# Kernel optimization log

Hardware: AMD Instinct MI355X
Metric: run time of the kernel (lower is better)

Reference implementation:

```python
import jax, jax.numpy as jnp
import numpy as np


def setup_inputs() -> dict:
    key = jax.random.key(0)
    heatmaps = jax.random.normal(key, (16, 24, 64, 64, 64), dtype=jnp.float32)
    return {"heatmaps": heatmaps}


def reference(heatmaps) -> jnp.ndarray:
    N, J, D, H, W = heatmaps.shape
    # softmax over the flattened D*H*W volume per (n, j)
    p = jax.nn.softmax(heatmaps.reshape(N, J, D * H * W), axis=2).reshape(N, J, D, H, W)
    x_maps = p.sum(axis=(2, 3))  # (N, J, W)
    y_maps = p.sum(axis=(2, 4))  # (N, J, H)
    z_maps = p.sum(axis=(3, 4))  # (N, J, D)
    w_idx = jnp.arange(W, dtype=p.dtype)
    h_idx = jnp.arange(H, dtype=p.dtype)
    d_idx = jnp.arange(D, dtype=p.dtype)
    x_preds = (x_maps * w_idx).sum(axis=2) / W - 0.5
    y_preds = (y_maps * h_idx).sum(axis=2) / H - 0.5
    z_preds = (z_maps * d_idx).sum(axis=2) / D - 0.5
    return jnp.stack((x_preds, y_preds, z_preds), axis=2)  # (N, J, 3)
```

## Files before the change

kernel.cpp:

```cpp
#include <hip/hip_runtime.h>

#define NJ   384
#define VOL  262144
#define CHUNKS 16
#define BLOCK 256
#define ELEMS_PER_BLOCK (VOL / CHUNKS)
#define VEC4_PER_BLOCK  (ELEMS_PER_BLOCK/4)
#define ITERS (VEC4_PER_BLOCK / BLOCK)


__global__ void jir_zero(float* __restrict__ acc) {
    int i = blockIdx.x * blockDim.x + threadIdx.x;
    if (i < NJ * 4) acc[i] = 0.0f;
}

__global__ __launch_bounds__(BLOCK) void jir_accum(const float* __restrict__ hm,
                                                   float* __restrict__ acc) {
    const int slice = blockIdx.x >> 4;
    const int chunk = blockIdx.x & 15;
    const int t = threadIdx.x;

    const float4* __restrict__ base =
        (const float4*)(hm + (size_t)slice * VOL + (size_t)chunk * ELEMS_PER_BLOCK);
    const int fbase = chunk * ELEMS_PER_BLOCK;

    float S = 0.f, Sx = 0.f, Sy = 0.f, Sz = 0.f;

#pragma unroll
    for (int i = 0; i < ITERS; ++i) {
        const int v = i * BLOCK + t;
        const float4 q = base[v];
        const int f = fbase + (v << 2);
        const float e0 = expf(q.x);
        const float e1 = expf(q.y);
        const float e2 = expf(q.z);
        const float e3 = expf(q.w);
        const float Se = (e0 + e1) + (e2 + e3);
        const float w0 = (float)(f & 63);
        const float hh = (float)((f >> 6) & 63);
        const float dd = (float)(f >> 12);
        S  += Se;
        Sx += w0 * Se + (e1 + 2.0f * e2 + 3.0f * e3);
        Sy += hh * Se;
        Sz += dd * Se;
    }

#pragma unroll
    for (int off = 32; off > 0; off >>= 1) {
        S  += __shfl_down(S,  off, 64);
        Sx += __shfl_down(Sx, off, 64);
        Sy += __shfl_down(Sy, off, 64);
        Sz += __shfl_down(Sz, off, 64);
    }

    __shared__ float red[BLOCK / 64][4];
    const int wid  = t >> 6;
    const int lane = t & 63;
    if (lane == 0) {
        red[wid][0] = S; red[wid][1] = Sx; red[wid][2] = Sy; red[wid][3] = Sz;
    }
    __syncthreads();
    if (t < 4) {
        const float v = red[0][t] + red[1][t] + red[2][t] + red[3][t];
        atomicAdd(&acc[slice * 4 + t], v);
    }
}

__global__ void jir_finalize(const float* __restrict__ acc, float* __restrict__ out) {
    int s = blockIdx.x * blockDim.x + threadIdx.x;
    if (s < NJ) {
        const float S  = acc[s * 4 + 0];
        const float Sx = acc[s * 4 + 1];
        const float Sy = acc[s * 4 + 2];
        const float Sz = acc[s * 4 + 3];
        const float inv = 1.0f / S;
        const float scale = inv * (1.0f / 64.0f);
        out[s * 3 + 0] = Sx * scale - 0.5f;
        out[s * 3 + 1] = Sy * scale - 0.5f;
        out[s * 3 + 2] = Sz * scale - 0.5f;
    }
}

extern "C" void kernel_launch(void* const* d_in, const int* in_sizes, int n_in,
                              void* d_out, int out_size, void* d_ws, size_t ws_size,
                              hipStream_t stream) {
    const float* hm = (const float*)d_in[0];
    float* out = (float*)d_out;
    float* acc = (float*)d_ws;

    jir_zero<<<(NJ * 4 + 255) / 256, 256, 0, stream>>>(acc);
    jir_accum<<<NJ * CHUNKS, BLOCK, 0, stream>>>(hm, acc);
    jir_finalize<<<(NJ + 191) / 192, 192, 0, stream>>>(acc, out);
}
```

Measured before the change: 519.4 us.

## Replace atomics with per-block partials, drop zero kernel, use fast exp

Each block now writes its four partial sums to a per-block workspace slot instead of atomically adding into a zeroed accumulator. The finalize kernel then sums the 16 chunk partials for each slice, so the separate zero-fill launch goes away. The accumulation loop switches to the hardware-approximate __expf, derives the w/h/d coordinates from the thread index and iteration number instead of recomputing them from the flat offset, and uses explicit FMAs. The kernel streams about 400MB and is expected to be bandwidth-bound, so the savings are mostly one fewer launch and less ALU work, at some cost in exp accuracy.

```diff
diff --git a/kernel.cpp b/kernel.cpp
--- a/kernel.cpp
+++ b/kernel.cpp
@@ -1,48 +1,43 @@
 #include <hip/hip_runtime.h>
 
-#define NJ   384
-#define VOL  262144
+
+#define NJ     384
+#define VOL    262144
 #define CHUNKS 16
-#define BLOCK 256
-#define ELEMS_PER_BLOCK (VOL / CHUNKS)
-#define VEC4_PER_BLOCK  (ELEMS_PER_BLOCK/4)
-#define ITERS (VEC4_PER_BLOCK / BLOCK)
-
-
-__global__ void jir_zero(float* __restrict__ acc) {
-    int i = blockIdx.x * blockDim.x + threadIdx.x;
-    if (i < NJ * 4) acc[i] = 0.0f;
-}
+#define BLOCK  256
+#define EPB    (VOL / CHUNKS)
+#define ITERS  (EPB / 4 / BLOCK)
 
 __global__ __launch_bounds__(BLOCK) void jir_accum(const float* __restrict__ hm,
-                                                   float* __restrict__ acc) {
+                                                   float4* __restrict__ partial) {
     const int slice = blockIdx.x >> 4;
     const int chunk = blockIdx.x & 15;
     const int t = threadIdx.x;
 
     const float4* __restrict__ base =
-        (const float4*)(hm + (size_t)slice * VOL + (size_t)chunk * ELEMS_PER_BLOCK);
-    const int fbase = chunk * ELEMS_PER_BLOCK;
+        (const float4*)(hm + (size_t)slice * VOL + (size_t)chunk * EPB) + t;
+
+    const float w0    = (float)((t & 15) << 2);
+    const float hbase = (float)(t >> 4);
+    const float dbase = (float)(chunk << 2);
 
     float S = 0.f, Sx = 0.f, Sy = 0.f, Sz = 0.f;
 
 #pragma unroll
     for (int i = 0; i < ITERS; ++i) {
-        const int v = i * BLOCK + t;
-        const float4 q = base[v];
-        const int f = fbase + (v << 2);
-        const float e0 = expf(q.x);
-        const float e1 = expf(q.y);
-        const float e2 = expf(q.z);
-        const float e3 = expf(q.w);
+        const float4 q = base[i * BLOCK];
+        const float e0 = __expf(q.x);
+        const float e1 = __expf(q.y);
+        const float e2 = __expf(q.z);
+        const float e3 = __expf(q.w);
         const float Se = (e0 + e1) + (e2 + e3);
-        const float w0 = (float)(f & 63);
-        const float hh = (float)((f >> 6) & 63);
-        const float dd = (float)(f >> 12);
+        const float hh = hbase + (float)((i & 3) << 4);
+        const float dd = dbase + (float)(i >> 2);
+        const float cx = fmaf(3.0f, e3, fmaf(2.0f, e2, e1));
         S  += Se;
-        Sx += w0 * Se + (e1 + 2.0f * e2 + 3.0f * e3);
-        Sy += hh * Se;
-        Sz += dd * Se;
+        Sx += fmaf(w0, Se, cx);
+        Sy  = fmaf(hh, Se, Sy);
+        Sz  = fmaf(dd, Se, Sz);
     }
 
 #pragma unroll
@@ -60,21 +55,27 @@
         red[wid][0] = S; red[wid][1] = Sx; red[wid][2] = Sy; red[wid][3] = Sz;
     }
     __syncthreads();
-    if (t < 4) {
-        const float v = red[0][t] + red[1][t] + red[2][t] + red[3][t];
-        atomicAdd(&acc[slice * 4 + t], v);
+    if (t == 0) {
+        float4 p;
+        p.x = (red[0][0] + red[1][0]) + (red[2][0] + red[3][0]);
+        p.y = (red[0][1] + red[1][1]) + (red[2][1] + red[3][1]);
+        p.z = (red[0][2] + red[1][2]) + (red[2][2] + red[3][2]);
+        p.w = (red[0][3] + red[1][3]) + (red[2][3] + red[3][3]);
+        partial[blockIdx.x] = p;
     }
 }
 
-__global__ void jir_finalize(const float* __restrict__ acc, float* __restrict__ out) {
-    int s = blockIdx.x * blockDim.x + threadIdx.x;
+__global__ void jir_finalize(const float4* __restrict__ partial,
+                             float* __restrict__ out) {
+    const int s = blockIdx.x * blockDim.x + threadIdx.x;
     if (s < NJ) {
-        const float S  = acc[s * 4 + 0];
-        const float Sx = acc[s * 4 + 1];
-        const float Sy = acc[s * 4 + 2];
-        const float Sz = acc[s * 4 + 3];
-        const float inv = 1.0f / S;
-        const float scale = inv * (1.0f / 64.0f);
+        float S = 0.f, Sx = 0.f, Sy = 0.f, Sz = 0.f;
+#pragma unroll
+        for (int c = 0; c < CHUNKS; ++c) {
+            const float4 p = partial[s * CHUNKS + c];
+            S += p.x; Sx += p.y; Sy += p.z; Sz += p.w;
+        }
+        const float scale = 1.0f / (S * 64.0f);
         out[s * 3 + 0] = Sx * scale - 0.5f;
         out[s * 3 + 1] = Sy * scale - 0.5f;
         out[s * 3 + 2] = Sz * scale - 0.5f;
@@ -86,9 +87,8 @@
                               hipStream_t stream) {
     const float* hm = (const float*)d_in[0];
     float* out = (float*)d_out;
-    float* acc = (float*)d_ws;
+    float4* partial = (float4*)d_ws;
 
-    jir_zero<<<(NJ * 4 + 255) / 256, 256, 0, stream>>>(acc);
-    jir_accum<<<NJ * CHUNKS, BLOCK, 0, stream>>>(hm, acc);
-    jir_finalize<<<(NJ + 191) / 192, 192, 0, stream>>>(acc, out);
+    jir_accum<<<NJ * CHUNKS, BLOCK, 0, stream>>>(hm, partial);
+    jir_finalize<<<2, 192, 0, stream>>>(partial, out);
 }
```

Result: no change. 512.9 us (-1.3%).
